# Kernel optimization log

Measured on AMD Instinct MI355X. Metric: run time of the kernel, lower is better.

The kernel has to match this reference:

```python
import jax, jax.numpy as jnp
import numpy as np

NUM_HEADS = 16


def setup_inputs() -> dict:
    key = jax.random.key(0)
    ks = jax.random.split(key, 3)
    B, S, E = 8, 1024, 1024
    x = jax.random.normal(ks[0], (B, S, E), dtype=jnp.float32)
    W_attn = jax.random.normal(ks[1], (E, 3 * E), dtype=jnp.float32) * (1.0 / np.sqrt(E))
    b_attn = jnp.zeros((3 * E,), dtype=jnp.float32)
    W_proj = jax.random.normal(ks[2], (E, E), dtype=jnp.float32) * (1.0 / np.sqrt(E))
    b_proj = jnp.zeros((E,), dtype=jnp.float32)
    return {"x": x, "W_attn": W_attn, "b_attn": b_attn, "W_proj": W_proj, "b_proj": b_proj}


def reference(x, W_attn, b_attn, W_proj, b_proj):
    # The module's blockwise "flash" loop implements exact causal softmax
    # attention (online softmax is mathematically identical); dropout is
    # inactive in eval mode.
    B, S, E = x.shape
    H = NUM_HEADS
    D = E // H
    qkv = x @ W_attn + b_attn  # [B,S,3E]
    q, k, v = jnp.split(qkv, 3, axis=-1)

    def split_heads(t):
        return t.reshape(B, S, H, D).transpose(0, 2, 1, 3)  # [B,H,S,D]

    q, k, v = split_heads(q), split_heads(k), split_heads(v)
    scores = jnp.einsum("bhqd,bhkd->bhqk", q, k) / jnp.sqrt(jnp.asarray(D, x.dtype))
    causal = jnp.tril(jnp.ones((S, S), dtype=bool))
    scores = jnp.where(causal, scores, -jnp.inf)
    probs = jax.nn.softmax(scores, axis=-1)
    out = jnp.einsum("bhqk,bhkd->bhqd", probs, v)  # [B,H,S,D]
    out = out.transpose(0, 2, 1, 3).reshape(B, S, E)
    return out @ W_proj + b_proj
```

## Files before the change

### kernel.cpp

```cpp
#include <hip/hip_runtime.h>
#include <hip/hip_bf16.h>
#include <stdint.h>

typedef unsigned short ushort_t;
typedef __attribute__((ext_vector_type(8))) __bf16 bf16x8;
typedef __attribute__((ext_vector_type(4))) float f32x4;

typedef const __attribute__((address_space(1))) uint32_t* gptr_t;
typedef __attribute__((address_space(3))) uint32_t* lptr_t;

__device__ __forceinline__ ushort_t f2bf(float f) {
  union { float f; uint32_t u; } x; x.f = f;
  uint32_t u = x.u;
  uint32_t r = (u + 0x7fffu + ((u >> 16) & 1u)) >> 16;
  return (ushort_t)r;
}

__device__ __forceinline__ uint32_t cvt_pk_bf16(float lo, float hi) {
  uint32_t r;
  asm("v_cvt_pk_bf16_f32 %0, %1, %2" : "=v"(r) : "v"(lo), "v"(hi));
  return r;
}

__device__ __forceinline__ void gload_lds16(const void* g, void* l) {
  __builtin_amdgcn_global_load_lds((gptr_t)g, (lptr_t)l, 16, 0, 0);
}

__global__ void prep(const float* __restrict__ x, ushort_t* __restrict__ xb,
                     const float* __restrict__ Wa, ushort_t* __restrict__ Wab,
                     const float* __restrict__ Wp, ushort_t* __restrict__ Wpb) {
  const int bid = blockIdx.x;
  if (bid < 8192) {
    const int idx = (bid * 256 + threadIdx.x) * 4;
    const float4 v = *(const float4*)(x + idx);
    ushort4 o;
    o.x = f2bf(v.x); o.y = f2bf(v.y); o.z = f2bf(v.z); o.w = f2bf(v.w);
    *(ushort4*)(xb + idx) = o;
  } else {
    __shared__ ushort_t t[32][33];
    const float* in; ushort_t* out; int N, n0, k0;
    const int K = 1024;
    if (bid < 11264) {
      const int i = bid - 8192; in = Wa; out = Wab; N = 3072;
      n0 = (i % 96) * 32; k0 = (i / 96) * 32;
    } else {
      const int i = bid - 11264; in = Wp; out = Wpb; N = 1024;
      n0 = (i % 32) * 32; k0 = (i / 32) * 32;
    }
    const int c = threadIdx.x & 31, r0 = threadIdx.x >> 5;
#pragma unroll
    for (int i = 0; i < 4; ++i) {
      const int r = r0 + i * 8;
      t[r][c] = f2bf(in[(size_t)(k0 + r) * N + n0 + c]);
    }
    __syncthreads();
#pragma unroll
    for (int i = 0; i < 4; ++i) {
      const int r = r0 + i * 8;
      out[(size_t)(n0 + r) * K + k0 + c] = t[c][r];
    }
  }
}

template<int MODE>
__global__ __launch_bounds__(256, 4) void gemm_bt(
    const ushort_t* __restrict__ A, const ushort_t* __restrict__ Bt,
    const float* __restrict__ bias,
    ushort_t* __restrict__ Cq, ushort_t* __restrict__ Ck, ushort_t* __restrict__ Cv,
    float* __restrict__ Cf,
    int M, int N, int K, float qscale)
{
  __shared__ ushort_t As[128 * 64];
  __shared__ ushort_t Bs[128 * 64];
  const int tid = threadIdx.x;
  const int w = tid >> 6, l = tid & 63;
  const int bm = blockIdx.y * 128, bn = blockIdx.x * 128;
  const int lr = l >> 3, lp = l & 7;
  const int l16 = l & 15, lhi = l >> 4;
  const int wm = (w >> 1) * 64, wn = (w & 1) * 64;

  f32x4 acc[4][4] = {};

  for (int kt = 0; kt < K; kt += 64) {
#pragma unroll
    for (int i = 0; i < 4; ++i) {
      const int ci = i * 4 + w;
      const int row = ci * 8 + lr;
      const int sc = (lp ^ (row & 7)) * 8;
      gload_lds16(A + (size_t)(bm + row) * K + kt + sc, &As[ci * 512]);
      gload_lds16(Bt + (size_t)(bn + row) * K + kt + sc, &Bs[ci * 512]);
    }
    __syncthreads();

    bf16x8 af[4][2], bfr[4][2];
#pragma unroll
    for (int mf = 0; mf < 4; ++mf) {
      const int row = wm + mf * 16 + l16;
#pragma unroll
      for (int kf = 0; kf < 2; ++kf) {
        const int ch = (lhi + kf * 4) ^ (row & 7);
        af[mf][kf] = *(const bf16x8*)((const char*)&As[row * 64] + ch * 16);
      }
    }
#pragma unroll
    for (int nf = 0; nf < 4; ++nf) {
      const int row = wn + nf * 16 + l16;
#pragma unroll
      for (int kf = 0; kf < 2; ++kf) {
        const int ch = (lhi + kf * 4) ^ (row & 7);
        bfr[nf][kf] = *(const bf16x8*)((const char*)&Bs[row * 64] + ch * 16);
      }
    }
#pragma unroll
    for (int kf = 0; kf < 2; ++kf)
#pragma unroll
      for (int mf = 0; mf < 4; ++mf)
#pragma unroll
        for (int nf = 0; nf < 4; ++nf)
          acc[mf][nf] = __builtin_amdgcn_mfma_f32_16x16x32_bf16(
              af[mf][kf], bfr[nf][kf], acc[mf][nf], 0, 0, 0);
    __syncthreads();
  }

#pragma unroll
  for (int mf = 0; mf < 4; ++mf) {
#pragma unroll
    for (int nf = 0; nf < 4; ++nf) {
      const int col = bn + wn + nf * 16 + l16;
      const float bv = bias[col];
#pragma unroll
      for (int r = 0; r < 4; ++r) {
        const int row = bm + wm + mf * 16 + lhi * 4 + r;
        float v = acc[mf][nf][r] + bv;
        if constexpr (MODE == 1) {
          Cf[(size_t)row * N + col] = v;
        } else {
          const int region = col >> 10;
          const int hcol = col & 1023;
          const int b_ = row >> 10, s_ = row & 1023;
          const int h_ = hcol >> 6, d_ = hcol & 63;
          if (region == 2) {
            Cv[((size_t)(b_ * 16 + h_) * 64 + d_) * 1024 + s_] = f2bf(v);
          } else {
            ushort_t* base = (region == 0) ? Cq : Ck;
            if (region == 0) v *= qscale;
            base[((size_t)(b_ * 16 + h_) * 1024 + s_) * 64 + d_] = f2bf(v);
          }
        }
      }
    }
  }
}

__global__ __launch_bounds__(256, 2) void attn_kernel(
    const ushort_t* __restrict__ Q, const ushort_t* __restrict__ Kk,
    const ushort_t* __restrict__ Vt, ushort_t* __restrict__ O)
{
  __shared__ ushort_t Pl[8][32 * 68];
  const int tid = threadIdx.x;
  const int w = tid >> 6, l = tid & 63;
  const int l16 = l & 15, lhi = l >> 4;

  const int bid = blockIdx.x;
  const int bh = ((bid >> 5) << 3) | (bid & 7);
  const int p  = (bid >> 3) & 3;
  const int qtH = 7 - p, qtL = p;
  const int qbH = qtH * 128 + w * 32;
  const int qbL = qtL * 128 + w * 32;
  const int ntH = (qbH >> 6) + 1;
  const int ntL = (qbL >> 6) + 1;
  const size_t hb = (size_t)bh * (1024 * 64);
  const int b_ = bh >> 4, h_ = bh & 15;

  bf16x8 qfH[2][2], qfL[2][2];
#pragma unroll
  for (int mf = 0; mf < 2; ++mf)
#pragma unroll
    for (int kf = 0; kf < 2; ++kf) {
      qfH[mf][kf] = *(const bf16x8*)(Q + hb + (size_t)(qbH + mf * 16 + l16) * 64 + kf * 32 + lhi * 8);
      qfL[mf][kf] = *(const bf16x8*)(Q + hb + (size_t)(qbL + mf * 16 + l16) * 64 + kf * 32 + lhi * 8);
    }

  f32x4 oH[2][4] = {}, oL[2][4] = {};
  float lsH[2] = {0.0f, 0.0f};
  float lsL[2] = {0.0f, 0.0f};
  char* const pbH = (char*)&Pl[w * 2 + 0][0];
  char* const pbL = (char*)&Pl[w * 2 + 1][0];

  for (int t = 0; t < ntH; ++t) {
    const int kv0 = t * 64;

    bf16x8 kb[4][2], vb[4][2];
#pragma unroll
    for (int nf = 0; nf < 4; ++nf)
#pragma unroll
      for (int kf = 0; kf < 2; ++kf) {
        kb[nf][kf] = *(const bf16x8*)(Kk + hb + (size_t)(kv0 + nf * 16 + l16) * 64 + kf * 32 + lhi * 8);
        vb[nf][kf] = *(const bf16x8*)(Vt + hb + (size_t)(nf * 16 + l16) * 1024 + kv0 + kf * 32 + lhi * 8);
      }

    auto half = [&](const bf16x8 (&qf)[2][2], f32x4 (&o)[2][4],
                    float (&l_run)[2],
                    const int qbase, char* const pbase) {
      f32x4 s[2][4] = {};
#pragma unroll
      for (int nf = 0; nf < 4; ++nf)
#pragma unroll
        for (int kf = 0; kf < 2; ++kf)
#pragma unroll
          for (int mf = 0; mf < 2; ++mf)
            s[mf][nf] = __builtin_amdgcn_mfma_f32_16x16x32_bf16(kb[nf][kf], qf[mf][kf], s[mf][nf], 0, 0, 0);

      if (kv0 + 63 > qbase) {
#pragma unroll
        for (int mf = 0; mf < 2; ++mf) {
          const int q = qbase + mf * 16 + l16;
#pragma unroll
          for (int nf = 0; nf < 4; ++nf)
#pragma unroll
            for (int r = 0; r < 4; ++r) {
              const int kv = kv0 + nf * 16 + lhi * 4 + r;
              if (kv > q) s[mf][nf][r] = -1e30f;
            }
        }
      }

#pragma unroll
      for (int mf = 0; mf < 2; ++mf) {
        float psum = 0.0f;
#pragma unroll
        for (int nf = 0; nf < 4; ++nf)
#pragma unroll
          for (int r = 0; r < 4; ++r) {
            const float pv = exp2f(s[mf][nf][r]);
            s[mf][nf][r] = pv;
            psum += pv;
          }
        l_run[mf] += psum;

        const int q = mf * 16 + l16;
#pragma unroll
        for (int nf = 0; nf < 4; ++nf) {
          const uint32_t u0 = cvt_pk_bf16(s[mf][nf][0], s[mf][nf][1]);
          const uint32_t u1 = cvt_pk_bf16(s[mf][nf][2], s[mf][nf][3]);
          *(uint2*)(pbase + q * 136 + nf * 32 + lhi * 8) = make_uint2(u0, u1);
        }
      }

#pragma unroll
      for (int mf = 0; mf < 2; ++mf) {
        const int q = mf * 16 + l16;
#pragma unroll
        for (int kf = 0; kf < 2; ++kf) {
          const bf16x8 pb = *(const bf16x8*)(pbase + q * 136 + kf * 64 + lhi * 16);
#pragma unroll
          for (int nf = 0; nf < 4; ++nf)
            o[mf][nf] = __builtin_amdgcn_mfma_f32_16x16x32_bf16(vb[nf][kf], pb, o[mf][nf], 0, 0, 0);
        }
      }
    };

    half(qfH, oH, lsH, qbH, pbH);
    if (t < ntL) half(qfL, oL, lsL, qbL, pbL);
  }

  auto epi = [&](f32x4 (&o)[2][4], float (&l_run)[2], const int qbase) {
#pragma unroll
    for (int mf = 0; mf < 2; ++mf) {
      float lt = l_run[mf];
      lt += __shfl_xor(lt, 16);
      lt += __shfl_xor(lt, 32);
      const float inv = 1.0f / lt;
      const int qrow = qbase + mf * 16 + l16;
      const size_t rb = ((size_t)(b_ * 1024 + qrow)) * 1024 + h_ * 64;
#pragma unroll
      for (int nf = 0; nf < 4; ++nf) {
        const uint32_t u0 = cvt_pk_bf16(o[mf][nf][0] * inv, o[mf][nf][1] * inv);
        const uint32_t u1 = cvt_pk_bf16(o[mf][nf][2] * inv, o[mf][nf][3] * inv);
        *(uint2*)(O + rb + nf * 16 + lhi * 4) = make_uint2(u0, u1);
      }
    }
  };
  epi(oH, lsH, qbH);
  epi(oL, lsL, qbL);
}

extern "C" void kernel_launch(void* const* d_in, const int* in_sizes, int n_in,
                              void* d_out, int out_size, void* d_ws, size_t ws_size,
                              hipStream_t stream) {
  const float* x      = (const float*)d_in[0];
  const float* W_attn = (const float*)d_in[1];
  const float* b_attn = (const float*)d_in[2];
  const float* W_proj = (const float*)d_in[3];
  const float* b_proj = (const float*)d_in[4];
  float* out = (float*)d_out;

  const int M = 8192;
  const int E = 1024, N3 = 3072;
  const size_t T = (size_t)M * E;

  char* p = (char*)d_ws;
  ushort_t* xb  = (ushort_t*)p; p += T * 2;
  ushort_t* Wab = (ushort_t*)p; p += (size_t)N3 * E * 2;
  ushort_t* Wpb = (ushort_t*)p; p += (size_t)E * E * 2;
  ushort_t* Qb  = (ushort_t*)p; p += T * 2;
  ushort_t* Kb  = (ushort_t*)p; p += T * 2;
  ushort_t* Vtb = (ushort_t*)p; p += T * 2;

  const float qscale = 0.125f * 1.4426950408889634f;

  prep<<<dim3(12288), dim3(256), 0, stream>>>(x, xb, W_attn, Wab, W_proj, Wpb);
  gemm_bt<2><<<dim3(N3 / 128, M / 128), dim3(256), 0, stream>>>(
      xb, Wab, b_attn, Qb, Kb, Vtb, nullptr, M, N3, E, qscale);
  attn_kernel<<<dim3(512), dim3(256), 0, stream>>>(Qb, Kb, Vtb, xb);
  gemm_bt<1><<<dim3(E / 128, M / 128), dim3(256), 0, stream>>>(
      xb, Wpb, b_proj, nullptr, nullptr, nullptr, out, M, E, E, 1.0f);
}
```

Baseline: 182.5 us.

## Split paired causal q-tiles into separate blocks and raise attention occupancy

Each attention block now handles a single 128-row query tile rather than a balanced high/low pair, which doubles the grid to 1024 blocks and halves LDS and register state per block so launch bounds can target 4 blocks per CU. A fixed QTMAP permutation interleaves short and long tiles across the block index to offset the causal load imbalance. The V loads are moved after the QK^T MFMAs so they overlap with compute. The cost is that each K/V load now serves one query tile instead of two, and the load balance depends on how the hardware schedules blocks.

Measured after the change: 223.0 us. 22.2% more time.

```diff
diff --git a/kernel.cpp b/kernel.cpp
--- a/kernel.cpp
+++ b/kernel.cpp
@@ -152,137 +152,125 @@
   }
 }
 
-__global__ __launch_bounds__(256, 2) void attn_kernel(
+__global__ __launch_bounds__(256, 4) void attn_kernel(
     const ushort_t* __restrict__ Q, const ushort_t* __restrict__ Kk,
     const ushort_t* __restrict__ Vt, ushort_t* __restrict__ O)
 {
-  __shared__ ushort_t Pl[8][32 * 68];
+  __shared__ ushort_t Pl[4][32 * 68];
   const int tid = threadIdx.x;
   const int w = tid >> 6, l = tid & 63;
   const int l16 = l & 15, lhi = l >> 4;
 
   const int bid = blockIdx.x;
-  const int bh = ((bid >> 5) << 3) | (bid & 7);
-  const int p  = (bid >> 3) & 3;
-  const int qtH = 7 - p, qtL = p;
-  const int qbH = qtH * 128 + w * 32;
-  const int qbL = qtL * 128 + w * 32;
-  const int ntH = (qbH >> 6) + 1;
-  const int ntL = (qbL >> 6) + 1;
+  const int bh = bid & 127;
+  constexpr int QTMAP[8] = {0, 2, 1, 3, 6, 4, 7, 5};
+  const int qt = QTMAP[bid >> 7];
+  const int qbase = qt * 128 + w * 32;
+  const int nt = (qbase >> 6) + 1;
   const size_t hb = (size_t)bh * (1024 * 64);
   const int b_ = bh >> 4, h_ = bh & 15;
-
-  bf16x8 qfH[2][2], qfL[2][2];
+  char* const pbase = (char*)&Pl[w][0];
+
+  bf16x8 qf[2][2];
 #pragma unroll
   for (int mf = 0; mf < 2; ++mf)
 #pragma unroll
-    for (int kf = 0; kf < 2; ++kf) {
-      qfH[mf][kf] = *(const bf16x8*)(Q + hb + (size_t)(qbH + mf * 16 + l16) * 64 + kf * 32 + lhi * 8);
-      qfL[mf][kf] = *(const bf16x8*)(Q + hb + (size_t)(qbL + mf * 16 + l16) * 64 + kf * 32 + lhi * 8);
-    }
-
-  f32x4 oH[2][4] = {}, oL[2][4] = {};
-  float lsH[2] = {0.0f, 0.0f};
-  float lsL[2] = {0.0f, 0.0f};
-  char* const pbH = (char*)&Pl[w * 2 + 0][0];
-  char* const pbL = (char*)&Pl[w * 2 + 1][0];
-
-  for (int t = 0; t < ntH; ++t) {
+    for (int kf = 0; kf < 2; ++kf)
+      qf[mf][kf] = *(const bf16x8*)(Q + hb + (size_t)(qbase + mf * 16 + l16) * 64 + kf * 32 + lhi * 8);
+
+  f32x4 o[2][4] = {};
+  float ls[2] = {0.0f, 0.0f};
+
+  for (int t = 0; t < nt; ++t) {
     const int kv0 = t * 64;
 
-    bf16x8 kb[4][2], vb[4][2];
+    bf16x8 kb[4][2];
 #pragma unroll
     for (int nf = 0; nf < 4; ++nf)
 #pragma unroll
+      for (int kf = 0; kf < 2; ++kf)
+        kb[nf][kf] = *(const bf16x8*)(Kk + hb + (size_t)(kv0 + nf * 16 + l16) * 64 + kf * 32 + lhi * 8);
+
+    f32x4 s[2][4] = {};
+#pragma unroll
+    for (int nf = 0; nf < 4; ++nf)
+#pragma unroll
+      for (int kf = 0; kf < 2; ++kf)
+#pragma unroll
+        for (int mf = 0; mf < 2; ++mf)
+          s[mf][nf] = __builtin_amdgcn_mfma_f32_16x16x32_bf16(kb[nf][kf], qf[mf][kf], s[mf][nf], 0, 0, 0);
+
+    bf16x8 vb[4][2];
+#pragma unroll
+    for (int nf = 0; nf < 4; ++nf)
+#pragma unroll
+      for (int kf = 0; kf < 2; ++kf)
+        vb[nf][kf] = *(const bf16x8*)(Vt + hb + (size_t)(nf * 16 + l16) * 1024 + kv0 + kf * 32 + lhi * 8);
+
+    if (kv0 + 63 > qbase) {
+#pragma unroll
+      for (int mf = 0; mf < 2; ++mf) {
+        const int q = qbase + mf * 16 + l16;
+#pragma unroll
+        for (int nf = 0; nf < 4; ++nf)
+#pragma unroll
+          for (int r = 0; r < 4; ++r) {
+            const int kv = kv0 + nf * 16 + lhi * 4 + r;
+            if (kv > q) s[mf][nf][r] = -1e30f;
+          }
+      }
+    }
+
+#pragma unroll
+    for (int mf = 0; mf < 2; ++mf) {
+      float psum = 0.0f;
+#pragma unroll
+      for (int nf = 0; nf < 4; ++nf)
+#pragma unroll
+        for (int r = 0; r < 4; ++r) {
+          const float pv = exp2f(s[mf][nf][r]);
+          s[mf][nf][r] = pv;
+          psum += pv;
+        }
+      ls[mf] += psum;
+
+      const int q = mf * 16 + l16;
+#pragma unroll
+      for (int nf = 0; nf < 4; ++nf) {
+        const uint32_t u0 = cvt_pk_bf16(s[mf][nf][0], s[mf][nf][1]);
+        const uint32_t u1 = cvt_pk_bf16(s[mf][nf][2], s[mf][nf][3]);
+        *(uint2*)(pbase + q * 136 + nf * 32 + lhi * 8) = make_uint2(u0, u1);
+      }
+    }
+
+#pragma unroll
+    for (int mf = 0; mf < 2; ++mf) {
+      const int q = mf * 16 + l16;
+#pragma unroll
       for (int kf = 0; kf < 2; ++kf) {
-        kb[nf][kf] = *(const bf16x8*)(Kk + hb + (size_t)(kv0 + nf * 16 + l16) * 64 + kf * 32 + lhi * 8);
-        vb[nf][kf] = *(const bf16x8*)(Vt + hb + (size_t)(nf * 16 + l16) * 1024 + kv0 + kf * 32 + lhi * 8);
-      }
-
-    auto half = [&](const bf16x8 (&qf)[2][2], f32x4 (&o)[2][4],
-                    float (&l_run)[2],
-                    const int qbase, char* const pbase) {
-      f32x4 s[2][4] = {};
-#pragma unroll
-      for (int nf = 0; nf < 4; ++nf)
-#pragma unroll
-        for (int kf = 0; kf < 2; ++kf)
-#pragma unroll
-          for (int mf = 0; mf < 2; ++mf)
-            s[mf][nf] = __builtin_amdgcn_mfma_f32_16x16x32_bf16(kb[nf][kf], qf[mf][kf], s[mf][nf], 0, 0, 0);
-
-      if (kv0 + 63 > qbase) {
-#pragma unroll
-        for (int mf = 0; mf < 2; ++mf) {
-          const int q = qbase + mf * 16 + l16;
-#pragma unroll
-          for (int nf = 0; nf < 4; ++nf)
-#pragma unroll
-            for (int r = 0; r < 4; ++r) {
-              const int kv = kv0 + nf * 16 + lhi * 4 + r;
-              if (kv > q) s[mf][nf][r] = -1e30f;
-            }
-        }
-      }
-
-#pragma unroll
-      for (int mf = 0; mf < 2; ++mf) {
-        float psum = 0.0f;
+        const bf16x8 pb = *(const bf16x8*)(pbase + q * 136 + kf * 64 + lhi * 16);
 #pragma unroll
         for (int nf = 0; nf < 4; ++nf)
-#pragma unroll
-          for (int r = 0; r < 4; ++r) {
-            const float pv = exp2f(s[mf][nf][r]);
-            s[mf][nf][r] = pv;
-            psum += pv;
-          }
-        l_run[mf] += psum;
-
-        const int q = mf * 16 + l16;
-#pragma unroll
-        for (int nf = 0; nf < 4; ++nf) {
-          const uint32_t u0 = cvt_pk_bf16(s[mf][nf][0], s[mf][nf][1]);
-          const uint32_t u1 = cvt_pk_bf16(s[mf][nf][2], s[mf][nf][3]);
-          *(uint2*)(pbase + q * 136 + nf * 32 + lhi * 8) = make_uint2(u0, u1);
-        }
-      }
-
-#pragma unroll
-      for (int mf = 0; mf < 2; ++mf) {
-        const int q = mf * 16 + l16;
-#pragma unroll
-        for (int kf = 0; kf < 2; ++kf) {
-          const bf16x8 pb = *(const bf16x8*)(pbase + q * 136 + kf * 64 + lhi * 16);
-#pragma unroll
-          for (int nf = 0; nf < 4; ++nf)
-            o[mf][nf] = __builtin_amdgcn_mfma_f32_16x16x32_bf16(vb[nf][kf], pb, o[mf][nf], 0, 0, 0);
-        }
-      }
-    };
-
-    half(qfH, oH, lsH, qbH, pbH);
-    if (t < ntL) half(qfL, oL, lsL, qbL, pbL);
-  }
-
-  auto epi = [&](f32x4 (&o)[2][4], float (&l_run)[2], const int qbase) {
-#pragma unroll
-    for (int mf = 0; mf < 2; ++mf) {
-      float lt = l_run[mf];
-      lt += __shfl_xor(lt, 16);
-      lt += __shfl_xor(lt, 32);
-      const float inv = 1.0f / lt;
-      const int qrow = qbase + mf * 16 + l16;
-      const size_t rb = ((size_t)(b_ * 1024 + qrow)) * 1024 + h_ * 64;
-#pragma unroll
-      for (int nf = 0; nf < 4; ++nf) {
-        const uint32_t u0 = cvt_pk_bf16(o[mf][nf][0] * inv, o[mf][nf][1] * inv);
-        const uint32_t u1 = cvt_pk_bf16(o[mf][nf][2] * inv, o[mf][nf][3] * inv);
-        *(uint2*)(O + rb + nf * 16 + lhi * 4) = make_uint2(u0, u1);
-      }
-    }
-  };
-  epi(oH, lsH, qbH);
-  epi(oL, lsL, qbL);
+          o[mf][nf] = __builtin_amdgcn_mfma_f32_16x16x32_bf16(vb[nf][kf], pb, o[mf][nf], 0, 0, 0);
+      }
+    }
+  }
+
+#pragma unroll
+  for (int mf = 0; mf < 2; ++mf) {
+    float lt = ls[mf];
+    lt += __shfl_xor(lt, 16);
+    lt += __shfl_xor(lt, 32);
+    const float inv = 1.0f / lt;
+    const int qrow = qbase + mf * 16 + l16;
+    const size_t rb = ((size_t)(b_ * 1024 + qrow)) * 1024 + h_ * 64;
+#pragma unroll
+    for (int nf = 0; nf < 4; ++nf) {
+      const uint32_t u0 = cvt_pk_bf16(o[mf][nf][0] * inv, o[mf][nf][1] * inv);
+      const uint32_t u1 = cvt_pk_bf16(o[mf][nf][2] * inv, o[mf][nf][3] * inv);
+      *(uint2*)(O + rb + nf * 16 + lhi * 4) = make_uint2(u0, u1);
+    }
+  }
 }
 
 extern "C" void kernel_launch(void* const* d_in, const int* in_sizes, int n_in,
@@ -312,7 +300,7 @@
   prep<<<dim3(12288), dim3(256), 0, stream>>>(x, xb, W_attn, Wab, W_proj, Wpb);
   gemm_bt<2><<<dim3(N3 / 128, M / 128), dim3(256), 0, stream>>>(
       xb, Wab, b_attn, Qb, Kb, Vtb, nullptr, M, N3, E, qscale);
-  attn_kernel<<<dim3(512), dim3(256), 0, stream>>>(Qb, Kb, Vtb, xb);
+  attn_kernel<<<dim3(1024), dim3(256), 0, stream>>>(Qb, Kb, Vtb, xb);
   gemm_bt<1><<<dim3(E / 128, M / 128), dim3(256), 0, stream>>>(
       xb, Wpb, b_proj, nullptr, nullptr, nullptr, out, M, E, E, 1.0f);
 }
```

## Halve per-wave query rows in attention and double the grid

Applied to the files above, without the earlier changes.

Each wave now handles 16 query rows per half instead of 32, and the block covers 64 query rows per paired tile. The grid grows from 512 to 1024 blocks, and per-thread registers and LDS shrink. The aim is more parallelism and occupancy on a 256-CU part, where 512 blocks underfill the machine. The cost is that each K/V fragment load from global memory is reused by half as many MFMAs, which doubles K/V traffic.

Result: slower. 252.3 us (+38.2%).

```diff
diff --git a/kernel.cpp b/kernel.cpp
--- a/kernel.cpp
+++ b/kernel.cpp
@@ -156,36 +156,33 @@
     const ushort_t* __restrict__ Q, const ushort_t* __restrict__ Kk,
     const ushort_t* __restrict__ Vt, ushort_t* __restrict__ O)
 {
-  __shared__ ushort_t Pl[8][32 * 68];
+  __shared__ ushort_t Pl[4][2][16 * 68];
   const int tid = threadIdx.x;
   const int w = tid >> 6, l = tid & 63;
   const int l16 = l & 15, lhi = l >> 4;
 
   const int bid = blockIdx.x;
-  const int bh = ((bid >> 5) << 3) | (bid & 7);
-  const int p  = (bid >> 3) & 3;
-  const int qtH = 7 - p, qtL = p;
-  const int qbH = qtH * 128 + w * 32;
-  const int qbL = qtL * 128 + w * 32;
+  const int bh = ((bid >> 6) << 3) | (bid & 7);
+  const int pb = (bid >> 3) & 7;
+  const int p = pb & 3, bsub = pb >> 2;
+  const int qbH = (7 - p) * 128 + bsub * 64 + w * 16;
+  const int qbL = p * 128 + bsub * 64 + w * 16;
   const int ntH = (qbH >> 6) + 1;
   const int ntL = (qbL >> 6) + 1;
   const size_t hb = (size_t)bh * (1024 * 64);
   const int b_ = bh >> 4, h_ = bh & 15;
 
-  bf16x8 qfH[2][2], qfL[2][2];
-#pragma unroll
-  for (int mf = 0; mf < 2; ++mf)
-#pragma unroll
-    for (int kf = 0; kf < 2; ++kf) {
-      qfH[mf][kf] = *(const bf16x8*)(Q + hb + (size_t)(qbH + mf * 16 + l16) * 64 + kf * 32 + lhi * 8);
-      qfL[mf][kf] = *(const bf16x8*)(Q + hb + (size_t)(qbL + mf * 16 + l16) * 64 + kf * 32 + lhi * 8);
-    }
-
-  f32x4 oH[2][4] = {}, oL[2][4] = {};
-  float lsH[2] = {0.0f, 0.0f};
-  float lsL[2] = {0.0f, 0.0f};
-  char* const pbH = (char*)&Pl[w * 2 + 0][0];
-  char* const pbL = (char*)&Pl[w * 2 + 1][0];
+  bf16x8 qfH[2], qfL[2];
+#pragma unroll
+  for (int kf = 0; kf < 2; ++kf) {
+    qfH[kf] = *(const bf16x8*)(Q + hb + (size_t)(qbH + l16) * 64 + kf * 32 + lhi * 8);
+    qfL[kf] = *(const bf16x8*)(Q + hb + (size_t)(qbL + l16) * 64 + kf * 32 + lhi * 8);
+  }
+
+  f32x4 oH[4] = {}, oL[4] = {};
+  float lsH = 0.0f, lsL = 0.0f;
+  char* const pbH = (char*)&Pl[w][0][0];
+  char* const pbL = (char*)&Pl[w][1][0];
 
   for (int t = 0; t < ntH; ++t) {
     const int kv0 = t * 64;
@@ -199,64 +196,50 @@
         vb[nf][kf] = *(const bf16x8*)(Vt + hb + (size_t)(nf * 16 + l16) * 1024 + kv0 + kf * 32 + lhi * 8);
       }
 
-    auto half = [&](const bf16x8 (&qf)[2][2], f32x4 (&o)[2][4],
-                    float (&l_run)[2],
+    auto half = [&](const bf16x8 (&qf)[2], f32x4 (&o)[4], float& l_run,
                     const int qbase, char* const pbase) {
-      f32x4 s[2][4] = {};
+      f32x4 s[4] = {};
 #pragma unroll
       for (int nf = 0; nf < 4; ++nf)
 #pragma unroll
         for (int kf = 0; kf < 2; ++kf)
-#pragma unroll
-          for (int mf = 0; mf < 2; ++mf)
-            s[mf][nf] = __builtin_amdgcn_mfma_f32_16x16x32_bf16(kb[nf][kf], qf[mf][kf], s[mf][nf], 0, 0, 0);
+          s[nf] = __builtin_amdgcn_mfma_f32_16x16x32_bf16(kb[nf][kf], qf[kf], s[nf], 0, 0, 0);
 
       if (kv0 + 63 > qbase) {
-#pragma unroll
-        for (int mf = 0; mf < 2; ++mf) {
-          const int q = qbase + mf * 16 + l16;
-#pragma unroll
-          for (int nf = 0; nf < 4; ++nf)
-#pragma unroll
-            for (int r = 0; r < 4; ++r) {
-              const int kv = kv0 + nf * 16 + lhi * 4 + r;
-              if (kv > q) s[mf][nf][r] = -1e30f;
-            }
+        const int q = qbase + l16;
+#pragma unroll
+        for (int nf = 0; nf < 4; ++nf)
+#pragma unroll
+          for (int r = 0; r < 4; ++r) {
+            const int kv = kv0 + nf * 16 + lhi * 4 + r;
+            if (kv > q) s[nf][r] = -1e30f;
+          }
+      }
+
+      float psum = 0.0f;
+#pragma unroll
+      for (int nf = 0; nf < 4; ++nf)
+#pragma unroll
+        for (int r = 0; r < 4; ++r) {
+          const float pv = exp2f(s[nf][r]);
+          s[nf][r] = pv;
+          psum += pv;
         }
-      }
-
-#pragma unroll
-      for (int mf = 0; mf < 2; ++mf) {
-        float psum = 0.0f;
+      l_run += psum;
+
+#pragma unroll
+      for (int nf = 0; nf < 4; ++nf) {
+        const uint32_t u0 = cvt_pk_bf16(s[nf][0], s[nf][1]);
+        const uint32_t u1 = cvt_pk_bf16(s[nf][2], s[nf][3]);
+        *(uint2*)(pbase + l16 * 136 + nf * 32 + lhi * 8) = make_uint2(u0, u1);
+      }
+
+#pragma unroll
+      for (int kf = 0; kf < 2; ++kf) {
+        const bf16x8 pb8 = *(const bf16x8*)(pbase + l16 * 136 + kf * 64 + lhi * 16);
 #pragma unroll
         for (int nf = 0; nf < 4; ++nf)
-#pragma unroll
-          for (int r = 0; r < 4; ++r) {
-            const float pv = exp2f(s[mf][nf][r]);
-            s[mf][nf][r] = pv;
-            psum += pv;
-          }
-        l_run[mf] += psum;
-
-        const int q = mf * 16 + l16;
-#pragma unroll
-        for (int nf = 0; nf < 4; ++nf) {
-          const uint32_t u0 = cvt_pk_bf16(s[mf][nf][0], s[mf][nf][1]);
-          const uint32_t u1 = cvt_pk_bf16(s[mf][nf][2], s[mf][nf][3]);
-          *(uint2*)(pbase + q * 136 + nf * 32 + lhi * 8) = make_uint2(u0, u1);
-        }
-      }
-
-#pragma unroll
-      for (int mf = 0; mf < 2; ++mf) {
-        const int q = mf * 16 + l16;
-#pragma unroll
-        for (int kf = 0; kf < 2; ++kf) {
-          const bf16x8 pb = *(const bf16x8*)(pbase + q * 136 + kf * 64 + lhi * 16);
-#pragma unroll
-          for (int nf = 0; nf < 4; ++nf)
-            o[mf][nf] = __builtin_amdgcn_mfma_f32_16x16x32_bf16(vb[nf][kf], pb, o[mf][nf], 0, 0, 0);
-        }
+          o[nf] = __builtin_amdgcn_mfma_f32_16x16x32_bf16(vb[nf][kf], pb8, o[nf], 0, 0, 0);
       }
     };
 
@@ -264,21 +247,18 @@
     if (t < ntL) half(qfL, oL, lsL, qbL, pbL);
   }
 
-  auto epi = [&](f32x4 (&o)[2][4], float (&l_run)[2], const int qbase) {
-#pragma unroll
-    for (int mf = 0; mf < 2; ++mf) {
-      float lt = l_run[mf];
-      lt += __shfl_xor(lt, 16);
-      lt += __shfl_xor(lt, 32);
-      const float inv = 1.0f / lt;
-      const int qrow = qbase + mf * 16 + l16;
-      const size_t rb = ((size_t)(b_ * 1024 + qrow)) * 1024 + h_ * 64;
-#pragma unroll
-      for (int nf = 0; nf < 4; ++nf) {
-        const uint32_t u0 = cvt_pk_bf16(o[mf][nf][0] * inv, o[mf][nf][1] * inv);
-        const uint32_t u1 = cvt_pk_bf16(o[mf][nf][2] * inv, o[mf][nf][3] * inv);
-        *(uint2*)(O + rb + nf * 16 + lhi * 4) = make_uint2(u0, u1);
-      }
+  auto epi = [&](f32x4 (&o)[4], float ls, const int qbase) {
+    float lt = ls;
+    lt += __shfl_xor(lt, 16);
+    lt += __shfl_xor(lt, 32);
+    const float inv = 1.0f / lt;
+    const int qrow = qbase + l16;
+    const size_t rb = ((size_t)(b_ * 1024 + qrow)) * 1024 + h_ * 64;
+#pragma unroll
+    for (int nf = 0; nf < 4; ++nf) {
+      const uint32_t u0 = cvt_pk_bf16(o[nf][0] * inv, o[nf][1] * inv);
+      const uint32_t u1 = cvt_pk_bf16(o[nf][2] * inv, o[nf][3] * inv);
+      *(uint2*)(O + rb + nf * 16 + lhi * 4) = make_uint2(u0, u1);
     }
   };
   epi(oH, lsH, qbH);
@@ -312,7 +292,7 @@
   prep<<<dim3(12288), dim3(256), 0, stream>>>(x, xb, W_attn, Wab, W_proj, Wpb);
   gemm_bt<2><<<dim3(N3 / 128, M / 128), dim3(256), 0, stream>>>(
       xb, Wab, b_attn, Qb, Kb, Vtb, nullptr, M, N3, E, qscale);
-  attn_kernel<<<dim3(512), dim3(256), 0, stream>>>(Qb, Kb, Vtb, xb);
+  attn_kernel<<<dim3(1024), dim3(256), 0, stream>>>(Qb, Kb, Vtb, xb);
   gemm_bt<1><<<dim3(E / 128, M / 128), dim3(256), 0, stream>>>(
       xb, Wpb, b_proj, nullptr, nullptr, nullptr, out, M, E, E, 1.0f);
 }
```

## Stage K/V tiles in double-buffered swizzled LDS shared across waves

Applied to the files above, without the earlier changes.

Replaces the per-wave direct global loads of K and V fragments with block-cooperative async global-to-LDS copies into two ping-pong buffers, prefetching the next tile while the current one is computed. An XOR swizzle on the chunk index is meant to avoid LDS bank conflicts on the fragment reads. Each K/V tile is now fetched once per block instead of once per wave, which cuts global/L2 traffic. In exchange it adds a block-wide barrier per iteration, extra LDS use that may lower occupancy, and a loop that always runs to the block's maximum tile count, so waves with fewer tiles sit idle at the barriers.

Result: faster. 172.6 us (-5.4%).

```diff
diff --git a/kernel.cpp b/kernel.cpp
--- a/kernel.cpp
+++ b/kernel.cpp
@@ -156,6 +156,8 @@
     const ushort_t* __restrict__ Q, const ushort_t* __restrict__ Kk,
     const ushort_t* __restrict__ Vt, ushort_t* __restrict__ O)
 {
+  __shared__ ushort_t Kl[2][64 * 64];
+  __shared__ ushort_t Vl[2][64 * 64];
   __shared__ ushort_t Pl[8][32 * 68];
   const int tid = threadIdx.x;
   const int w = tid >> 6, l = tid & 63;
@@ -169,8 +171,23 @@
   const int qbL = qtL * 128 + w * 32;
   const int ntH = (qbH >> 6) + 1;
   const int ntL = (qbL >> 6) + 1;
+  const int NT  = 2 * qtH + 2;
   const size_t hb = (size_t)bh * (1024 * 64);
   const int b_ = bh >> 4, h_ = bh & 15;
+
+  const int srow = l >> 3;
+  const int sch  = l & 7;
+  const int schs = sch ^ srow;
+
+  auto STAGE = [&](int buf, int t) {
+    const int kv0 = t * 64;
+#pragma unroll
+    for (int j = 0; j < 2; ++j) {
+      const int row = j * 32 + w * 8 + srow;
+      gload_lds16(Kk + hb + (size_t)(kv0 + row) * 64 + schs * 8, &Kl[buf][row * 64 + sch * 8]);
+      gload_lds16(Vt + hb + (size_t)row * 1024 + kv0 + schs * 8, &Vl[buf][row * 64 + sch * 8]);
+    }
+  };
 
   bf16x8 qfH[2][2], qfL[2][2];
 #pragma unroll
@@ -187,29 +204,29 @@
   char* const pbH = (char*)&Pl[w * 2 + 0][0];
   char* const pbL = (char*)&Pl[w * 2 + 1][0];
 
-  for (int t = 0; t < ntH; ++t) {
+  STAGE(0, 0);
+  __syncthreads();
+
+  for (int t = 0; t < NT; ++t) {
+    const int buf = t & 1;
+    if (t + 1 < NT) STAGE(buf ^ 1, t + 1);
     const int kv0 = t * 64;
 
-    bf16x8 kb[4][2], vb[4][2];
-#pragma unroll
-    for (int nf = 0; nf < 4; ++nf)
-#pragma unroll
-      for (int kf = 0; kf < 2; ++kf) {
-        kb[nf][kf] = *(const bf16x8*)(Kk + hb + (size_t)(kv0 + nf * 16 + l16) * 64 + kf * 32 + lhi * 8);
-        vb[nf][kf] = *(const bf16x8*)(Vt + hb + (size_t)(nf * 16 + l16) * 1024 + kv0 + kf * 32 + lhi * 8);
-      }
-
-    auto half = [&](const bf16x8 (&qf)[2][2], f32x4 (&o)[2][4],
-                    float (&l_run)[2],
+    auto half = [&](const bf16x8 (&qf)[2][2], f32x4 (&o)[2][4], float (&l_run)[2],
                     const int qbase, char* const pbase) {
       f32x4 s[2][4] = {};
 #pragma unroll
-      for (int nf = 0; nf < 4; ++nf)
-#pragma unroll
-        for (int kf = 0; kf < 2; ++kf)
+      for (int nf = 0; nf < 4; ++nf) {
+        const int row = nf * 16 + l16;
+#pragma unroll
+        for (int kf = 0; kf < 2; ++kf) {
+          const int bo = (kf * 64 + lhi * 16) ^ ((row & 7) << 4);
+          const bf16x8 kb = *(const bf16x8*)((const char*)&Kl[buf][row * 64] + bo);
 #pragma unroll
           for (int mf = 0; mf < 2; ++mf)
-            s[mf][nf] = __builtin_amdgcn_mfma_f32_16x16x32_bf16(kb[nf][kf], qf[mf][kf], s[mf][nf], 0, 0, 0);
+            s[mf][nf] = __builtin_amdgcn_mfma_f32_16x16x32_bf16(kb, qf[mf][kf], s[mf][nf], 0, 0, 0);
+        }
+      }
 
       if (kv0 + 63 > qbase) {
 #pragma unroll
@@ -248,20 +265,29 @@
       }
 
 #pragma unroll
-      for (int mf = 0; mf < 2; ++mf) {
-        const int q = mf * 16 + l16;
-#pragma unroll
-        for (int kf = 0; kf < 2; ++kf) {
-          const bf16x8 pb = *(const bf16x8*)(pbase + q * 136 + kf * 64 + lhi * 16);
+      for (int kf = 0; kf < 2; ++kf) {
+        bf16x8 vbf[4];
+#pragma unroll
+        for (int nf = 0; nf < 4; ++nf) {
+          const int row = nf * 16 + l16;
+          const int bo = (kf * 64 + lhi * 16) ^ ((row & 7) << 4);
+          vbf[nf] = *(const bf16x8*)((const char*)&Vl[buf][row * 64] + bo);
+        }
+#pragma unroll
+        for (int mf = 0; mf < 2; ++mf) {
+          const int q = mf * 16 + l16;
+          const bf16x8 pb8 = *(const bf16x8*)(pbase + q * 136 + kf * 64 + lhi * 16);
 #pragma unroll
           for (int nf = 0; nf < 4; ++nf)
-            o[mf][nf] = __builtin_amdgcn_mfma_f32_16x16x32_bf16(vb[nf][kf], pb, o[mf][nf], 0, 0, 0);
+            o[mf][nf] = __builtin_amdgcn_mfma_f32_16x16x32_bf16(vbf[nf], pb8, o[mf][nf], 0, 0, 0);
         }
       }
     };
 
-    half(qfH, oH, lsH, qbH, pbH);
+    if (t < ntH) half(qfH, oH, lsH, qbH, pbH);
     if (t < ntL) half(qfL, oL, lsL, qbL, pbL);
+
+    __syncthreads();
   }
 
   auto epi = [&](f32x4 (&o)[2][4], float (&l_run)[2], const int qbase) {
```
